# Kernel tuning notes

Hardware: AMD Instinct MI355X
Metric: run time of the kernel (lower is better)

## Reference

```python
import jax, jax.numpy as jnp
import numpy as np

B, S, D, H, DK, DV = 4, 2048, 512, 8, 64, 64
LN_EPS = 1e-5


def setup_inputs() -> dict:
    key = jax.random.key(0)
    ks = jax.random.split(key, 8)
    scale = 1.0 / np.sqrt(D)
    return {
        "input_Q": jax.random.normal(ks[0], (B, S, D), jnp.float32),
        "input_K": jax.random.normal(ks[1], (B, S, D), jnp.float32),
        "input_V": jax.random.normal(ks[2], (B, S, D), jnp.float32),
        "attn_mask": jax.random.randint(ks[3], (B, S, S), 0, 2).astype(jnp.bool_),
        "W_Q": jax.random.normal(ks[4], (D, H * DK), jnp.float32) * scale,
        "W_K": jax.random.normal(ks[5], (D, H * DK), jnp.float32) * scale,
        "W_V": jax.random.normal(ks[6], (D, H * DV), jnp.float32) * scale,
        "W_fc": jax.random.normal(ks[7], (H * DV, D), jnp.float32) * scale,
        "ln_gamma": jnp.ones((D,), jnp.float32),
        "ln_beta": jnp.zeros((D,), jnp.float32),
    }


def reference(input_Q, input_K, input_V, attn_mask, W_Q, W_K, W_V, W_fc, ln_gamma, ln_beta):
    b, s, _ = input_Q.shape
    # projections -> [b, h, s, d]
    Q = (input_Q @ W_Q).reshape(b, s, H, DK).transpose(0, 2, 1, 3)
    K = (input_K @ W_K).reshape(b, s, H, DK).transpose(0, 2, 1, 3)
    V = (input_V @ W_V).reshape(b, s, H, DV).transpose(0, 2, 1, 3)
    # full [b, h, q, k] score matrix (faithful to explicit matmul->mask->softmax)
    scores = jnp.einsum("bhqd,bhkd->bhqk", Q, K) / np.sqrt(DK).astype(np.float32)
    scores = jnp.where(attn_mask[:, None, :, :], -jnp.inf, scores)
    attn = jax.nn.softmax(scores, axis=-1)
    context = jnp.einsum("bhqk,bhkd->bhqd", attn, V)  # [b, h, s, dv]
    context = context.transpose(0, 2, 1, 3).reshape(b, s, H * DV)
    output = context @ W_fc  # dropout is identity in eval / p=0
    x = output + input_Q  # residual
    mean = jnp.mean(x, axis=-1, keepdims=True)
    var = jnp.var(x, axis=-1, keepdims=True)
    return (x - mean) * jax.lax.rsqrt(var + LN_EPS) * ln_gamma + ln_beta
```

## Files before the change

kernel.cpp:

```cpp
#include <hip/hip_runtime.h>


#define B_ 4
#define S_ 2048
#define D_ 512
#define H_ 8

typedef __attribute__((ext_vector_type(8))) short short8_t;
typedef __attribute__((ext_vector_type(4))) short short4_t;
typedef __attribute__((ext_vector_type(4))) float f32x4;
typedef __attribute__((ext_vector_type(16))) float f32x16;
typedef __attribute__((ext_vector_type(4))) unsigned u32x4;
typedef __attribute__((ext_vector_type(2))) unsigned u32x2;

__device__ __forceinline__ short f2bf(float f) {
    unsigned u = __builtin_bit_cast(unsigned, f);
    u += 0x7fff + ((u >> 16) & 1);
    return (short)(u >> 16);
}

__device__ __forceinline__ unsigned pk2(float a, float b) {
    return __builtin_amdgcn_perm(__builtin_bit_cast(unsigned, b),
                                 __builtin_bit_cast(unsigned, a), 0x07060302u);
}

__device__ __forceinline__ float bf2f(short v) {
    return __builtin_bit_cast(float, (unsigned)((unsigned short)v) << 16);
}

__global__ __launch_bounds__(256) void pack_mask_kernel(const void* __restrict__ mask,
                                                        unsigned* __restrict__ bits) {
    __shared__ int isBool;
    if (threadIdx.x == 0) isBool = 0;
    __syncthreads();
    const unsigned char* bytes = (const unsigned char*)mask;
    if (threadIdx.x < 64) {
        if (bytes[threadIdx.x * 4 + 1] | bytes[threadIdx.x * 4 + 2] | bytes[threadIdx.x * 4 + 3])
            isBool = 1;
    }
    __syncthreads();
    int t = blockIdx.x * 256 + threadIdx.x;
    int half = t & 1, q = (t >> 1) & 2047, kt = (t >> 12) & 31, b = t >> 17;
    size_t src = ((size_t)(b * 2048 + q)) * 2048 + kt * 64 + half * 32;
    unsigned v = 0;
    if (isBool) {
        const unsigned char* p = bytes + src;
        #pragma unroll
        for (int i = 0; i < 32; ++i) v |= (p[i] ? 1u : 0u) << i;
    } else {
        const int* p = (const int*)mask + src;
        #pragma unroll
        for (int i = 0; i < 32; ++i) v |= (p[i] ? 1u : 0u) << i;
    }
    bits[(((size_t)(b * 32 + kt)) * 2048 + q) * 2 + half] = ~v;
}

__global__ __launch_bounds__(256) void proj_kernel(
    const float* __restrict__ inQ, const float* __restrict__ inK, const float* __restrict__ inV,
    const float* __restrict__ wq, const float* __restrict__ wk, const float* __restrict__ wv,
    short* __restrict__ Qp, short* __restrict__ Kp, short* __restrict__ Vp) {
    __shared__ short As[64 * 64];
    __shared__ short Bs[64 * 64];
    const int z = blockIdx.z;
    const float* A = (z == 0) ? inQ : ((z == 1) ? inK : inV);
    const float* W = (z == 0) ? wq : ((z == 1) ? wk : wv);
    short* O = (z == 0) ? Qp : ((z == 1) ? Kp : Vp);
    const float scale = (z == 0) ? 0.125f * 1.44269504f : 1.0f;
    const int bm = blockIdx.x * 64, bn = blockIdx.y * 64;
    const int tid = threadIdx.x, lane = tid & 63, wv_ = tid >> 6;
    const int wm = (wv_ >> 1) * 32, wn = (wv_ & 1) * 32;
    f32x4 acc[2][2] = {};

    for (int k0 = 0; k0 < 512; k0 += 64) {
        __syncthreads();
        #pragma unroll
        for (int it = 0; it < 4; ++it) {
            int g = tid + it * 256;
            int r = g >> 4, c4 = (g & 15) * 4;
            f32x4 v = *(const f32x4*)(A + (size_t)(bm + r) * 512 + k0 + c4);
            u32x2 u = { pk2(v.x, v.y), pk2(v.z, v.w) };
            *(u32x2*)((char*)As + r * 128 + ((c4 * 2) ^ ((r & 7) << 4))) = u;
        }
        #pragma unroll
        for (int it = 0; it < 2; ++it) {
            int g = tid + it * 256;
            int kp = g >> 4, n4 = (g & 15) * 4;
            const float* wrow = W + (size_t)(k0 + 2 * kp) * 512 + bn + n4;
            f32x4 va = *(const f32x4*)(wrow);
            f32x4 vb = *(const f32x4*)(wrow + 512);
            #pragma unroll
            for (int j = 0; j < 4; ++j) {
                int n = n4 + j;
                *(unsigned*)((char*)Bs + n * 128 + ((4 * kp) ^ ((n & 7) << 4))) = pk2(va[j], vb[j]);
            }
        }
        __syncthreads();
        #pragma unroll
        for (int kk = 0; kk < 2; ++kk) {
            short8_t af[2], bfr[2];
            #pragma unroll
            for (int rf = 0; rf < 2; ++rf) {
                int row = wm + rf * 16 + (lane & 15);
                af[rf] = *(const short8_t*)((const char*)As + row * 128 +
                          ((kk * 64 + ((lane >> 4) * 16)) ^ ((row & 7) << 4)));
            }
            #pragma unroll
            for (int cf = 0; cf < 2; ++cf) {
                int n = wn + cf * 16 + (lane & 15);
                bfr[cf] = *(const short8_t*)((const char*)Bs + n * 128 +
                           ((kk * 64 + ((lane >> 4) * 16)) ^ ((n & 7) << 4)));
            }
            __builtin_amdgcn_s_setprio(1);
            #pragma unroll
            for (int rf = 0; rf < 2; ++rf)
                #pragma unroll
                for (int cf = 0; cf < 2; ++cf)
                    acc[rf][cf] = __builtin_amdgcn_mfma_f32_16x16x32_bf16(af[rf], bfr[cf], acc[rf][cf], 0, 0, 0);
            __builtin_amdgcn_s_setprio(0);
        }
    }

    if (z == 0) {
        #pragma unroll
        for (int rf = 0; rf < 2; ++rf)
            #pragma unroll
            for (int cf = 0; cf < 2; ++cf)
                #pragma unroll
                for (int r = 0; r < 4; ++r) {
                    int row = bm + wm + rf * 16 + (lane >> 4) * 4 + r;
                    int col = bn + wn + cf * 16 + (lane & 15);
                    size_t idx = ((((size_t)(row >> 11)) * 8 + (col >> 6)) * 2048 + (row & 2047)) * 64 + (col & 63);
                    O[idx] = f2bf(acc[rf][cf][r] * scale);
                }
    } else {
        const int bb = bm >> 11, kt = (bm & 2047) >> 6, hh = bn >> 6;
        const size_t base = ((size_t)(bb * 8 + hh)) * 131072 + (size_t)kt * 4096;
        __syncthreads();
        if (z == 1) {
            #pragma unroll
            for (int rf = 0; rf < 2; ++rf)
                #pragma unroll
                for (int cf = 0; cf < 2; ++cf)
                    #pragma unroll
                    for (int r = 0; r < 4; ++r) {
                        int key = wm + rf * 16 + (lane >> 4) * 4 + r;
                        int dk = wn + cf * 16 + (lane & 15);
                        *(short*)((char*)As + key * 128 + ((dk * 2) ^ ((key & 7) << 4))) = f2bf(acc[rf][cf][r]);
                    }
        } else {
            #pragma unroll
            for (int rf = 0; rf < 2; ++rf)
                #pragma unroll
                for (int cf = 0; cf < 2; ++cf)
                    #pragma unroll
                    for (int r = 0; r < 4; ++r) {
                        int key = wm + rf * 16 + (lane >> 4) * 4 + r;
                        int dv = wn + cf * 16 + (lane & 15);
                        *(short*)((char*)As + dv * 128 + ((key * 2) ^ ((dv & 7) << 4))) = f2bf(acc[rf][cf][r]);
                    }
        }
        __syncthreads();
        #pragma unroll
        for (int it = 0; it < 2; ++it) {
            int u = tid + it * 256;
            int blk = u >> 7, h2 = (u >> 6) & 1, rr = u & 63;
            short8_t v8 = *(const short8_t*)((const char*)As + rr * 128 +
                           ((blk * 32 + h2 * 16) ^ ((rr & 7) << 4)));
            *(short8_t*)(O + base + (size_t)u * 8) = v8;
        }
    }
}

__global__ __launch_bounds__(256, 4) void attn_kernel(
    const short* __restrict__ Qp, const short* __restrict__ Kf, const short* __restrict__ Vf,
    const unsigned long long* __restrict__ mbits64, short* __restrict__ ctx) {
    __shared__ short Pw_all[4][2048];
    __shared__ float l_lds[4][32];
    int flat = blockIdx.x + 64 * (blockIdx.y + 8 * blockIdx.z);
    int x8 = flat & 7, s = flat >> 3;
    int bh = x8 * 4 + (s >> 6);
    int qi = s & 63;
    const int b = bh >> 3, h = bh & 7;
    const int tid = threadIdx.x, lane = tid & 63, w = tid >> 6;
    const int hi = lane >> 5, r31 = lane & 31;
    const size_t hb = ((size_t)bh) * 131072;
    const int qw = qi * 32;
    const int q_lane = qw + r31;
    const int t_beg = w * 8, t_end = t_beg + 8;

    short8_t qf[4];
    #pragma unroll
    for (int ks = 0; ks < 4; ++ks)
        qf[ks] = *(const short8_t*)(Qp + hb + (size_t)q_lane * 64 + ks * 16 + hi * 8);

    const short* Kb_ = Kf + hb + hi * 512 + r31 * 8;
    const short* Vb_ = Vf + hb + hi * 512 + r31 * 8;
    const unsigned long long* mrow = mbits64 + (size_t)b * 65536 + q_lane;

    f32x16 o0 = {}, o1 = {};
    float l_run = 0.f;

    for (int kt = t_beg; kt < t_end; ++kt) {
        const short* kp = Kb_ + (size_t)kt * 4096;
        unsigned long long wmx = mrow[(size_t)kt * 2048] >> (hi * 4);
        unsigned kl = (unsigned)wmx, kh = (unsigned)(wmx >> 32);

        f32x16 s0 = {}, s1 = {};
        __builtin_amdgcn_s_setprio(1);
        #pragma unroll
        for (int ks = 0; ks < 4; ++ks) {
            short8_t kf0 = *(const short8_t*)(kp + ks * 1024);
            short8_t kf1 = *(const short8_t*)(kp + ks * 1024 + 256);
            s0 = __builtin_amdgcn_mfma_f32_32x32x16_bf16(kf0, qf[ks], s0, 0, 0, 0);
            s1 = __builtin_amdgcn_mfma_f32_32x32x16_bf16(kf1, qf[ks], s1, 0, 0, 0);
        }
        __builtin_amdgcn_s_setprio(0);

        float r4[4] = { 0.f, 0.f, 0.f, 0.f };
        #pragma unroll
        for (int reg = 0; reg < 16; ++reg) {
            const int pos = (reg >> 2) * 8 + (reg & 3);
            float e0 = __builtin_amdgcn_exp2f(s0[reg]);
            float e1 = __builtin_amdgcn_exp2f(s1[reg]);
            unsigned k0b = (unsigned)__builtin_amdgcn_sbfe((int)kl, pos, 1);
            unsigned k1b = (unsigned)__builtin_amdgcn_sbfe((int)kh, pos, 1);
            float v0 = __builtin_bit_cast(float, __builtin_bit_cast(unsigned, e0) & k0b);
            float v1 = __builtin_bit_cast(float, __builtin_bit_cast(unsigned, e1) & k1b);
            s0[reg] = v0; s1[reg] = v1;
            r4[reg & 3] += v0 + v1;
        }
        float rs = (r4[0] + r4[1]) + (r4[2] + r4[3]);
        rs += __shfl_xor(rs, 32, 64);
        l_run += rs;

        const short* vp = Vb_ + (size_t)kt * 4096;
        #pragma unroll
        for (int kb = 0; kb < 4; ++kb) {
            const int e = (kb & 1) * 8;
            unsigned c0 = (kb < 2) ? pk2(s0[e + 0], s0[e + 1]) : pk2(s1[e + 0], s1[e + 1]);
            unsigned c1 = (kb < 2) ? pk2(s0[e + 2], s0[e + 3]) : pk2(s1[e + 2], s1[e + 3]);
            unsigned c2 = (kb < 2) ? pk2(s0[e + 4], s0[e + 5]) : pk2(s1[e + 4], s1[e + 5]);
            unsigned c3 = (kb < 2) ? pk2(s0[e + 6], s0[e + 7]) : pk2(s1[e + 6], s1[e + 7]);
#if __has_builtin(__builtin_amdgcn_permlane32_swap)
            u32x2 r02 = __builtin_amdgcn_permlane32_swap(c0, c2, false, false);
            u32x2 r13 = __builtin_amdgcn_permlane32_swap(c1, c3, false, false);
            u32x4 bw = { r02[0], r13[0], r02[1], r13[1] };
#else
            unsigned x0 = __shfl_xor(c0, 32, 64), x1 = __shfl_xor(c1, 32, 64);
            unsigned x2 = __shfl_xor(c2, 32, 64), x3 = __shfl_xor(c3, 32, 64);
            unsigned w0 = hi ? x2 : c0, w1 = hi ? x3 : c1;
            unsigned w2 = hi ? c2 : x0, w3 = hi ? c3 : x1;
            u32x4 bw = { w0, w1, w2, w3 };
#endif
            short8_t pb = __builtin_bit_cast(short8_t, bw);
            short8_t vf0 = *(const short8_t*)(vp + kb * 1024);
            short8_t vf1 = *(const short8_t*)(vp + kb * 1024 + 256);
            __builtin_amdgcn_s_setprio(1);
            o0 = __builtin_amdgcn_mfma_f32_32x32x16_bf16(vf0, pb, o0, 0, 0, 0);
            o1 = __builtin_amdgcn_mfma_f32_32x32x16_bf16(vf1, pb, o1, 0, 0, 0);
            __builtin_amdgcn_s_setprio(0);
        }
    }

    float invl = 1.0f / fmaxf(l_run, 1e-37f);
    short* Pw = Pw_all[w];
    #pragma unroll
    for (int dvb = 0; dvb < 2; ++dvb)
        #pragma unroll
        for (int g = 0; g < 4; ++g) {
            short4_t v4;
            #pragma unroll
            for (int t = 0; t < 4; ++t) {
                float val = (dvb ? o1[g * 4 + t] : o0[g * 4 + t]) * invl;
                v4[t] = f2bf(val);
            }
            int dv0 = dvb * 32 + g * 8 + hi * 4;
            *(short4_t*)((char*)Pw + r31 * 128 + ((dv0 * 2) ^ ((r31 & 7) << 4))) = v4;
        }
    if (hi == 0) l_lds[w][r31] = l_run;
    __syncthreads();

    const int q = tid >> 3, j = tid & 7;
    float acc8[8] = {};
    float wsum = 0.f;
    #pragma unroll
    for (int ww = 0; ww < 4; ++ww) {
        float lw = l_lds[ww][q];
        wsum += lw;
        short8_t v8 = *(const short8_t*)((const char*)Pw_all[ww] + q * 128 + ((j * 16) ^ ((q & 7) << 4)));
        #pragma unroll
        for (int e = 0; e < 8; ++e)
            acc8[e] += bf2f(v8[e]) * lw;
    }
    float inv = 1.f / fmaxf(wsum, 1e-37f);
    u32x4 ov = { pk2(acc8[0] * inv, acc8[1] * inv), pk2(acc8[2] * inv, acc8[3] * inv),
                 pk2(acc8[4] * inv, acc8[5] * inv), pk2(acc8[6] * inv, acc8[7] * inv) };
    *(short8_t*)(ctx + ((size_t)(b * 2048 + qw + q)) * 512 + h * 64 + j * 8) =
        __builtin_bit_cast(short8_t, ov);
}

__global__ __launch_bounds__(256) void fc_kernel(
    const short* __restrict__ ctx, const float* __restrict__ wfc,
    const float* __restrict__ inQ, float* __restrict__ xbuf) {
    __shared__ short As[64 * 64];
    __shared__ short Bs[64 * 64];
    const int bm = blockIdx.x * 64, bn = blockIdx.y * 64;
    const int tid = threadIdx.x, lane = tid & 63, wv_ = tid >> 6;
    const int wm = (wv_ >> 1) * 32, wn = (wv_ & 1) * 32;
    f32x4 acc[2][2] = {};

    for (int k0 = 0; k0 < 512; k0 += 64) {
        __syncthreads();
        #pragma unroll
        for (int it = 0; it < 2; ++it) {
            int g = tid + it * 256;
            int r = g >> 3, c8 = (g & 7) * 8;
            short8_t v = *(const short8_t*)(ctx + (size_t)(bm + r) * 512 + k0 + c8);
            *(short8_t*)((char*)As + r * 128 + ((c8 * 2) ^ ((r & 7) << 4))) = v;
        }
        #pragma unroll
        for (int it = 0; it < 2; ++it) {
            int g = tid + it * 256;
            int kp = g >> 4, n4 = (g & 15) * 4;
            const float* wrow = wfc + (size_t)(k0 + 2 * kp) * 512 + bn + n4;
            f32x4 va = *(const f32x4*)(wrow);
            f32x4 vb = *(const f32x4*)(wrow + 512);
            #pragma unroll
            for (int j = 0; j < 4; ++j) {
                int n = n4 + j;
                *(unsigned*)((char*)Bs + n * 128 + ((4 * kp) ^ ((n & 7) << 4))) = pk2(va[j], vb[j]);
            }
        }
        __syncthreads();
        #pragma unroll
        for (int kk = 0; kk < 2; ++kk) {
            short8_t af[2], bfr[2];
            #pragma unroll
            for (int rf = 0; rf < 2; ++rf) {
                int row = wm + rf * 16 + (lane & 15);
                af[rf] = *(const short8_t*)((const char*)As + row * 128 +
                          ((kk * 64 + ((lane >> 4) * 16)) ^ ((row & 7) << 4)));
            }
            #pragma unroll
            for (int cf = 0; cf < 2; ++cf) {
                int n = wn + cf * 16 + (lane & 15);
                bfr[cf] = *(const short8_t*)((const char*)Bs + n * 128 +
                           ((kk * 64 + ((lane >> 4) * 16)) ^ ((n & 7) << 4)));
            }
            __builtin_amdgcn_s_setprio(1);
            #pragma unroll
            for (int rf = 0; rf < 2; ++rf)
                #pragma unroll
                for (int cf = 0; cf < 2; ++cf)
                    acc[rf][cf] = __builtin_amdgcn_mfma_f32_16x16x32_bf16(af[rf], bfr[cf], acc[rf][cf], 0, 0, 0);
            __builtin_amdgcn_s_setprio(0);
        }
    }
    #pragma unroll
    for (int rf = 0; rf < 2; ++rf)
        #pragma unroll
        for (int cf = 0; cf < 2; ++cf)
            #pragma unroll
            for (int r = 0; r < 4; ++r) {
                int row = bm + wm + rf * 16 + (lane >> 4) * 4 + r;
                int col = bn + wn + cf * 16 + (lane & 15);
                size_t idx = (size_t)row * 512 + col;
                xbuf[idx] = acc[rf][cf][r] + inQ[idx];
            }
}

__global__ __launch_bounds__(256) void ln_kernel(
    const float* __restrict__ x, const float* __restrict__ gamma,
    const float* __restrict__ beta, float* __restrict__ out) {
    __shared__ float rs[4], rq[4];
    const int row = blockIdx.x, tid = threadIdx.x;
    const int w = tid >> 6, lane = tid & 63;
    float2 v = *(const float2*)(x + (size_t)row * 512 + tid * 2);
    float s = v.x + v.y, sq = v.x * v.x + v.y * v.y;
    #pragma unroll
    for (int off = 32; off; off >>= 1) {
        s += __shfl_down(s, off, 64);
        sq += __shfl_down(sq, off, 64);
    }
    if (lane == 0) { rs[w] = s; rq[w] = sq; }
    __syncthreads();
    if (tid == 0) {
        rs[0] = rs[0] + rs[1] + rs[2] + rs[3];
        rq[0] = rq[0] + rq[1] + rq[2] + rq[3];
    }
    __syncthreads();
    float mean = rs[0] * (1.f / 512.f);
    float var = rq[0] * (1.f / 512.f) - mean * mean;
    float inv = rsqrtf(var + 1e-5f);
    int c0 = tid * 2;
    float2 g = *(const float2*)(gamma + c0);
    float2 be = *(const float2*)(beta + c0);
    float2 o;
    o.x = (v.x - mean) * inv * g.x + be.x;
    o.y = (v.y - mean) * inv * g.y + be.y;
    *(float2*)(out + (size_t)row * 512 + c0) = o;
}

extern "C" void kernel_launch(void* const* d_in, const int* in_sizes, int n_in,
                              void* d_out, int out_size, void* d_ws, size_t ws_size,
                              hipStream_t stream) {
    const float* inQ = (const float*)d_in[0];
    const float* inK = (const float*)d_in[1];
    const float* inV = (const float*)d_in[2];
    const void* mask = d_in[3];
    const float* wq = (const float*)d_in[4];
    const float* wk = (const float*)d_in[5];
    const float* wv = (const float*)d_in[6];
    const float* wfc = (const float*)d_in[7];
    const float* gamma = (const float*)d_in[8];
    const float* beta = (const float*)d_in[9];
    float* out = (float*)d_out;
    char* ws = (char*)d_ws;

    short* Qp = (short*)(ws);
    short* Kp = (short*)(ws + (size_t)(8 << 20));
    short* Vp = (short*)(ws + (size_t)(16 << 20));
    short* ctx = (short*)(ws + (size_t)(24 << 20));
    unsigned* mbits = (unsigned*)(ws + (size_t)(32 << 20));
    float* xbuf = (float*)(ws);

    pack_mask_kernel<<<2048, 256, 0, stream>>>(mask, mbits);
    proj_kernel<<<dim3(128, 8, 3), 256, 0, stream>>>(inQ, inK, inV, wq, wk, wv, Qp, Kp, Vp);
    attn_kernel<<<dim3(64, 8, 4), 256, 0, stream>>>(
        Qp, Kp, Vp, (const unsigned long long*)mbits, ctx);
    fc_kernel<<<dim3(128, 8, 1), 256, 0, stream>>>(ctx, wfc, inQ, xbuf);
    ln_kernel<<<8192, 256, 0, stream>>>(xbuf, gamma, beta, out);
}
```

Measured before the change: 139.3 us.

## Software-pipeline attention QK and PV phases, vectorize mask packing, one-wave LayerNorm rows

The attention loop is unrolled and software-pipelined so the QK^T MFMAs for the next key tile are issued while softmax and PV run on the current tile. Two score buffers are kept live, and the per-tile cross-half row-sum shuffle is deferred to a single shuffle at the end. The occupancy hint drops from 4 to 3 blocks per CU to make room for the extra registers, and the setprio hints are removed. Mask packing now reads 16-byte vectors and uses a bit-trick nibble extraction, and LayerNorm handles one row per wave with float4 loads and no LDS or barriers.

After: 204.3 us. 46.6% more time.

```diff
diff --git a/kernel.cpp b/kernel.cpp
--- a/kernel.cpp
+++ b/kernel.cpp
@@ -26,6 +26,12 @@
 
 __device__ __forceinline__ float bf2f(short v) {
     return __builtin_bit_cast(float, (unsigned)((unsigned short)v) << 16);
+}
+
+__device__ __forceinline__ unsigned nib4(unsigned w4) {
+    unsigned t = (w4 & 0x7f7f7f7fu) + 0x7f7f7f7fu;
+    t |= w4;
+    return (((t >> 7) & 0x01010101u) * 0x01020408u) >> 24;
 }
 
 __global__ __launch_bounds__(256) void pack_mask_kernel(const void* __restrict__ mask,
@@ -44,13 +50,17 @@
     size_t src = ((size_t)(b * 2048 + q)) * 2048 + kt * 64 + half * 32;
     unsigned v = 0;
     if (isBool) {
-        const unsigned char* p = bytes + src;
-        #pragma unroll
-        for (int i = 0; i < 32; ++i) v |= (p[i] ? 1u : 0u) << i;
+        const u32x4* p = (const u32x4*)(bytes + src);
+        u32x4 w0 = p[0], w1 = p[1];
+        v = nib4(w0[0]) | (nib4(w0[1]) << 4) | (nib4(w0[2]) << 8) | (nib4(w0[3]) << 12) |
+            (nib4(w1[0]) << 16) | (nib4(w1[1]) << 20) | (nib4(w1[2]) << 24) | (nib4(w1[3]) << 28);
     } else {
-        const int* p = (const int*)mask + src;
-        #pragma unroll
-        for (int i = 0; i < 32; ++i) v |= (p[i] ? 1u : 0u) << i;
+        const u32x4* p = (const u32x4*)((const int*)mask + src);
+        #pragma unroll
+        for (int j = 0; j < 8; ++j) {
+            u32x4 wv = p[j];
+            v |= ((wv[0] ? 1u : 0u) | (wv[1] ? 2u : 0u) | (wv[2] ? 4u : 0u) | (wv[3] ? 8u : 0u)) << (j * 4);
+        }
     }
     bits[(((size_t)(b * 32 + kt)) * 2048 + q) * 2 + half] = ~v;
 }
@@ -171,7 +181,70 @@
     }
 }
 
-__global__ __launch_bounds__(256, 4) void attn_kernel(
+
+#define QK_PHASE(KT, S0, S1, WM) do {                                          \
+    const short* kp_ = Kb_ + (size_t)(KT) * 4096;                              \
+    (WM) = mrow[(size_t)(KT) * 2048] >> (hi * 4);                              \
+    (S0) = vzero; (S1) = vzero;                                                \
+    _Pragma("unroll")                                                          \
+    for (int ks_ = 0; ks_ < 4; ++ks_) {                                        \
+        short8_t kf0_ = *(const short8_t*)(kp_ + ks_ * 1024);                  \
+        short8_t kf1_ = *(const short8_t*)(kp_ + ks_ * 1024 + 256);            \
+        (S0) = __builtin_amdgcn_mfma_f32_32x32x16_bf16(kf0_, qf[ks_], (S0), 0, 0, 0); \
+        (S1) = __builtin_amdgcn_mfma_f32_32x32x16_bf16(kf1_, qf[ks_], (S1), 0, 0, 0); \
+    }                                                                          \
+} while (0)
+
+#if __has_builtin(__builtin_amdgcn_permlane32_swap)
+#define REPACK(C0, C1, C2, C3, BW) do {                                        \
+    u32x2 r02_ = __builtin_amdgcn_permlane32_swap((C0), (C2), false, false);   \
+    u32x2 r13_ = __builtin_amdgcn_permlane32_swap((C1), (C3), false, false);   \
+    (BW) = (u32x4){ r02_[0], r13_[0], r02_[1], r13_[1] };                      \
+} while (0)
+#else
+#define REPACK(C0, C1, C2, C3, BW) do {                                        \
+    unsigned x0_ = __shfl_xor((C0), 32, 64), x1_ = __shfl_xor((C1), 32, 64);   \
+    unsigned x2_ = __shfl_xor((C2), 32, 64), x3_ = __shfl_xor((C3), 32, 64);   \
+    (BW) = (u32x4){ hi ? x2_ : (C0), hi ? x3_ : (C1),                          \
+                    hi ? (C2) : x0_, hi ? (C3) : x1_ };                        \
+} while (0)
+#endif
+
+#define SMPV_PHASE(KT, S0, S1, WM) do {                                        \
+    unsigned kl_ = (unsigned)(WM), kh_ = (unsigned)((WM) >> 32);               \
+    float r4_[4] = { 0.f, 0.f, 0.f, 0.f };                                     \
+    _Pragma("unroll")                                                          \
+    for (int reg_ = 0; reg_ < 16; ++reg_) {                                    \
+        const int pos_ = (reg_ >> 2) * 8 + (reg_ & 3);                         \
+        float e0_ = __builtin_amdgcn_exp2f((S0)[reg_]);                        \
+        float e1_ = __builtin_amdgcn_exp2f((S1)[reg_]);                        \
+        unsigned k0_ = (unsigned)__builtin_amdgcn_sbfe((int)kl_, pos_, 1);     \
+        unsigned k1_ = (unsigned)__builtin_amdgcn_sbfe((int)kh_, pos_, 1);     \
+        float v0_ = __builtin_bit_cast(float, __builtin_bit_cast(unsigned, e0_) & k0_); \
+        float v1_ = __builtin_bit_cast(float, __builtin_bit_cast(unsigned, e1_) & k1_); \
+        (S0)[reg_] = v0_; (S1)[reg_] = v1_;                                    \
+        r4_[reg_ & 3] += v0_ + v1_;                                            \
+    }                                                                          \
+    l_run += (r4_[0] + r4_[1]) + (r4_[2] + r4_[3]);                            \
+    const short* vp_ = Vb_ + (size_t)(KT) * 4096;                              \
+    _Pragma("unroll")                                                          \
+    for (int kb_ = 0; kb_ < 4; ++kb_) {                                        \
+        const int e_ = (kb_ & 1) * 8;                                          \
+        unsigned c0_ = (kb_ < 2) ? pk2((S0)[e_ + 0], (S0)[e_ + 1]) : pk2((S1)[e_ + 0], (S1)[e_ + 1]); \
+        unsigned c1_ = (kb_ < 2) ? pk2((S0)[e_ + 2], (S0)[e_ + 3]) : pk2((S1)[e_ + 2], (S1)[e_ + 3]); \
+        unsigned c2_ = (kb_ < 2) ? pk2((S0)[e_ + 4], (S0)[e_ + 5]) : pk2((S1)[e_ + 4], (S1)[e_ + 5]); \
+        unsigned c3_ = (kb_ < 2) ? pk2((S0)[e_ + 6], (S0)[e_ + 7]) : pk2((S1)[e_ + 6], (S1)[e_ + 7]); \
+        u32x4 bw_;                                                             \
+        REPACK(c0_, c1_, c2_, c3_, bw_);                                       \
+        short8_t pb_ = __builtin_bit_cast(short8_t, bw_);                      \
+        short8_t vf0_ = *(const short8_t*)(vp_ + kb_ * 1024);                  \
+        short8_t vf1_ = *(const short8_t*)(vp_ + kb_ * 1024 + 256);            \
+        o0 = __builtin_amdgcn_mfma_f32_32x32x16_bf16(vf0_, pb_, o0, 0, 0, 0);  \
+        o1 = __builtin_amdgcn_mfma_f32_32x32x16_bf16(vf1_, pb_, o1, 0, 0, 0);  \
+    }                                                                          \
+} while (0)
+
+__global__ __launch_bounds__(256, 3) void attn_kernel(
     const short* __restrict__ Qp, const short* __restrict__ Kf, const short* __restrict__ Vf,
     const unsigned long long* __restrict__ mbits64, short* __restrict__ ctx) {
     __shared__ short Pw_all[4][2048];
@@ -186,7 +259,7 @@
     const size_t hb = ((size_t)bh) * 131072;
     const int qw = qi * 32;
     const int q_lane = qw + r31;
-    const int t_beg = w * 8, t_end = t_beg + 8;
+    const int t_beg = w * 8;
 
     short8_t qf[4];
     #pragma unroll
@@ -197,70 +270,21 @@
     const short* Vb_ = Vf + hb + hi * 512 + r31 * 8;
     const unsigned long long* mrow = mbits64 + (size_t)b * 65536 + q_lane;
 
-    f32x16 o0 = {}, o1 = {};
+    const f32x16 vzero = {};
+    f32x16 o0 = vzero, o1 = vzero;
+    f32x16 sA0, sA1, sB0, sB1;
+    unsigned long long wmA, wmB;
     float l_run = 0.f;
 
-    for (int kt = t_beg; kt < t_end; ++kt) {
-        const short* kp = Kb_ + (size_t)kt * 4096;
-        unsigned long long wmx = mrow[(size_t)kt * 2048] >> (hi * 4);
-        unsigned kl = (unsigned)wmx, kh = (unsigned)(wmx >> 32);
-
-        f32x16 s0 = {}, s1 = {};
-        __builtin_amdgcn_s_setprio(1);
-        #pragma unroll
-        for (int ks = 0; ks < 4; ++ks) {
-            short8_t kf0 = *(const short8_t*)(kp + ks * 1024);
-            short8_t kf1 = *(const short8_t*)(kp + ks * 1024 + 256);
-            s0 = __builtin_amdgcn_mfma_f32_32x32x16_bf16(kf0, qf[ks], s0, 0, 0, 0);
-            s1 = __builtin_amdgcn_mfma_f32_32x32x16_bf16(kf1, qf[ks], s1, 0, 0, 0);
-        }
-        __builtin_amdgcn_s_setprio(0);
-
-        float r4[4] = { 0.f, 0.f, 0.f, 0.f };
-        #pragma unroll
-        for (int reg = 0; reg < 16; ++reg) {
-            const int pos = (reg >> 2) * 8 + (reg & 3);
-            float e0 = __builtin_amdgcn_exp2f(s0[reg]);
-            float e1 = __builtin_amdgcn_exp2f(s1[reg]);
-            unsigned k0b = (unsigned)__builtin_amdgcn_sbfe((int)kl, pos, 1);
-            unsigned k1b = (unsigned)__builtin_amdgcn_sbfe((int)kh, pos, 1);
-            float v0 = __builtin_bit_cast(float, __builtin_bit_cast(unsigned, e0) & k0b);
-            float v1 = __builtin_bit_cast(float, __builtin_bit_cast(unsigned, e1) & k1b);
-            s0[reg] = v0; s1[reg] = v1;
-            r4[reg & 3] += v0 + v1;
-        }
-        float rs = (r4[0] + r4[1]) + (r4[2] + r4[3]);
-        rs += __shfl_xor(rs, 32, 64);
-        l_run += rs;
-
-        const short* vp = Vb_ + (size_t)kt * 4096;
-        #pragma unroll
-        for (int kb = 0; kb < 4; ++kb) {
-            const int e = (kb & 1) * 8;
-            unsigned c0 = (kb < 2) ? pk2(s0[e + 0], s0[e + 1]) : pk2(s1[e + 0], s1[e + 1]);
-            unsigned c1 = (kb < 2) ? pk2(s0[e + 2], s0[e + 3]) : pk2(s1[e + 2], s1[e + 3]);
-            unsigned c2 = (kb < 2) ? pk2(s0[e + 4], s0[e + 5]) : pk2(s1[e + 4], s1[e + 5]);
-            unsigned c3 = (kb < 2) ? pk2(s0[e + 6], s0[e + 7]) : pk2(s1[e + 6], s1[e + 7]);
-#if __has_builtin(__builtin_amdgcn_permlane32_swap)
-            u32x2 r02 = __builtin_amdgcn_permlane32_swap(c0, c2, false, false);
-            u32x2 r13 = __builtin_amdgcn_permlane32_swap(c1, c3, false, false);
-            u32x4 bw = { r02[0], r13[0], r02[1], r13[1] };
-#else
-            unsigned x0 = __shfl_xor(c0, 32, 64), x1 = __shfl_xor(c1, 32, 64);
-            unsigned x2 = __shfl_xor(c2, 32, 64), x3 = __shfl_xor(c3, 32, 64);
-            unsigned w0 = hi ? x2 : c0, w1 = hi ? x3 : c1;
-            unsigned w2 = hi ? c2 : x0, w3 = hi ? c3 : x1;
-            u32x4 bw = { w0, w1, w2, w3 };
-#endif
-            short8_t pb = __builtin_bit_cast(short8_t, bw);
-            short8_t vf0 = *(const short8_t*)(vp + kb * 1024);
-            short8_t vf1 = *(const short8_t*)(vp + kb * 1024 + 256);
-            __builtin_amdgcn_s_setprio(1);
-            o0 = __builtin_amdgcn_mfma_f32_32x32x16_bf16(vf0, pb, o0, 0, 0, 0);
-            o1 = __builtin_amdgcn_mfma_f32_32x32x16_bf16(vf1, pb, o1, 0, 0, 0);
-            __builtin_amdgcn_s_setprio(0);
-        }
-    }
+    QK_PHASE(t_beg, sA0, sA1, wmA);
+    #pragma unroll
+    for (int i = 0; i < 4; ++i) {
+        QK_PHASE(t_beg + 2 * i + 1, sB0, sB1, wmB);
+        SMPV_PHASE(t_beg + 2 * i, sA0, sA1, wmA);
+        if (i < 3) QK_PHASE(t_beg + 2 * i + 2, sA0, sA1, wmA);
+        SMPV_PHASE(t_beg + 2 * i + 1, sB0, sB1, wmB);
+    }
+    l_run += __shfl_xor(l_run, 32, 64);
 
     float invl = 1.0f / fmaxf(l_run, 1e-37f);
     short* Pw = Pw_all[w];
@@ -372,33 +396,37 @@
 __global__ __launch_bounds__(256) void ln_kernel(
     const float* __restrict__ x, const float* __restrict__ gamma,
     const float* __restrict__ beta, float* __restrict__ out) {
-    __shared__ float rs[4], rq[4];
-    const int row = blockIdx.x, tid = threadIdx.x;
-    const int w = tid >> 6, lane = tid & 63;
-    float2 v = *(const float2*)(x + (size_t)row * 512 + tid * 2);
-    float s = v.x + v.y, sq = v.x * v.x + v.y * v.y;
+    const int w = threadIdx.x >> 6, lane = threadIdx.x & 63;
+    const int row = blockIdx.x * 4 + w;
+    const f32x4* xr = (const f32x4*)(x + (size_t)row * 512);
+    f32x4 a = xr[lane * 2], bb = xr[lane * 2 + 1];
+    float s = (a.x + a.y) + (a.z + a.w) + (bb.x + bb.y) + (bb.z + bb.w);
+    float sq = a.x * a.x + a.y * a.y + a.z * a.z + a.w * a.w +
+               bb.x * bb.x + bb.y * bb.y + bb.z * bb.z + bb.w * bb.w;
     #pragma unroll
     for (int off = 32; off; off >>= 1) {
-        s += __shfl_down(s, off, 64);
-        sq += __shfl_down(sq, off, 64);
-    }
-    if (lane == 0) { rs[w] = s; rq[w] = sq; }
-    __syncthreads();
-    if (tid == 0) {
-        rs[0] = rs[0] + rs[1] + rs[2] + rs[3];
-        rq[0] = rq[0] + rq[1] + rq[2] + rq[3];
-    }
-    __syncthreads();
-    float mean = rs[0] * (1.f / 512.f);
-    float var = rq[0] * (1.f / 512.f) - mean * mean;
+        s += __shfl_xor(s, off, 64);
+        sq += __shfl_xor(sq, off, 64);
+    }
+    float mean = s * (1.f / 512.f);
+    float var = sq * (1.f / 512.f) - mean * mean;
     float inv = rsqrtf(var + 1e-5f);
-    int c0 = tid * 2;
-    float2 g = *(const float2*)(gamma + c0);
-    float2 be = *(const float2*)(beta + c0);
-    float2 o;
-    o.x = (v.x - mean) * inv * g.x + be.x;
-    o.y = (v.y - mean) * inv * g.y + be.y;
-    *(float2*)(out + (size_t)row * 512 + c0) = o;
+    const f32x4* gr = (const f32x4*)gamma;
+    const f32x4* br = (const f32x4*)beta;
+    f32x4 g0 = gr[lane * 2], g1 = gr[lane * 2 + 1];
+    f32x4 b0 = br[lane * 2], b1 = br[lane * 2 + 1];
+    f32x4 o0, o1;
+    o0.x = (a.x - mean) * inv * g0.x + b0.x;
+    o0.y = (a.y - mean) * inv * g0.y + b0.y;
+    o0.z = (a.z - mean) * inv * g0.z + b0.z;
+    o0.w = (a.w - mean) * inv * g0.w + b0.w;
+    o1.x = (bb.x - mean) * inv * g1.x + b1.x;
+    o1.y = (bb.y - mean) * inv * g1.y + b1.y;
+    o1.z = (bb.z - mean) * inv * g1.z + b1.z;
+    o1.w = (bb.w - mean) * inv * g1.w + b1.w;
+    f32x4* orow = (f32x4*)(out + (size_t)row * 512);
+    orow[lane * 2] = o0;
+    orow[lane * 2 + 1] = o1;
 }
 
 extern "C" void kernel_launch(void* const* d_in, const int* in_sizes, int n_in,
@@ -429,5 +457,5 @@
     attn_kernel<<<dim3(64, 8, 4), 256, 0, stream>>>(
         Qp, Kp, Vp, (const unsigned long long*)mbits, ctx);
     fc_kernel<<<dim3(128, 8, 1), 256, 0, stream>>>(ctx, wfc, inQ, xbuf);
-    ln_kernel<<<8192, 256, 0, stream>>>(xbuf, gamma, beta, out);
-}
+    ln_kernel<<<2048, 256, 0, stream>>>(xbuf, gamma, beta, out);
+}
```
